# Kernel tuning notes

Hardware: AMD Instinct MI355X
Metric: run time of the kernel (lower is better)

Reference implementation:

```python
import jax, jax.numpy as jnp
import numpy as np
import math

N, T, D, H = 64, 128, 512, 1024

def setup_inputs() -> dict:
    key = jax.random.key(0)
    ks = jax.random.split(key, 5)
    x = jax.random.normal(ks[0], (N, T, D), dtype=jnp.float32)
    A = jax.random.normal(ks[1], (N, H, 4, 4), dtype=jnp.float32)
    Wx = jax.random.normal(ks[2], (D, 4 * H), dtype=jnp.float32) / math.sqrt(D)
    Wh = jax.random.normal(ks[3], (H, 4 * H), dtype=jnp.float32) / math.sqrt(H)
    Wattn = jax.random.normal(ks[4], (H, 4 * H), dtype=jnp.float32) / math.sqrt(H)
    b = jnp.zeros((4 * H,), dtype=jnp.float32)
    return {"x": x, "A": A, "Wx": Wx, "Wh": Wh, "Wattn": Wattn, "b": b}

def reference(x, A, Wx, Wh, Wattn, b):
    n, t, d = x.shape
    h_dim = A.shape[1]
    L = A.shape[2] * A.shape[3]  # 16 spatial locations
    Af = A.reshape(n, h_dim, L)                      # (N, H, 16)
    h0 = jnp.mean(Af, axis=-1)                       # mean over 4x4 -> (N, H)
    c0 = h0
    inv_sqrt_h = 1.0 / math.sqrt(h_dim)

    def step(carry, xt):
        prev_h, prev_c = carry
        # scaled dot-product attention over 16 locations
        scores = jnp.einsum('nh,nhl->nl', prev_h, Af) * inv_sqrt_h  # (N, 16)
        w = jax.nn.softmax(scores, axis=1)
        attn = jnp.einsum('nhl,nl->nh', Af, w)                      # (N, H)
        # LSTM gates
        a = xt @ Wx + prev_h @ Wh + attn @ Wattn + b                # (N, 4H)
        i, f, o, g = jnp.split(a, 4, axis=1)
        i, f, o = jax.nn.sigmoid(i), jax.nn.sigmoid(f), jax.nn.sigmoid(o)
        g = jnp.tanh(g)
        next_c = f * prev_c + i * g
        next_h = o * jnp.tanh(next_c)
        return (next_h, next_c), next_h

    xs = jnp.swapaxes(x, 0, 1)                       # (T, N, D)
    _, hs = jax.lax.scan(step, (h0, c0), xs)         # hs: (T, N, H)
    return jnp.swapaxes(hs, 0, 1)                    # (N, T, H)
```

## Files before the change

kernel.cpp:

```cpp
#include <hip/hip_runtime.h>
#include <stdint.h>


#define Tt 128
#define FH 4096
#define RING_D 32

typedef __bf16 bf8 __attribute__((ext_vector_type(8)));
typedef float f4 __attribute__((ext_vector_type(4)));
typedef short s8v __attribute__((ext_vector_type(8)));
typedef unsigned long long ull;

__device__ __forceinline__ float bf2f(unsigned short u) {
    union { unsigned u32; float f; } x; x.u32 = ((unsigned)u) << 16; return x.f;
}
__device__ __forceinline__ unsigned short f2bf(float f) {
    union { float f32; unsigned u; } x; x.f32 = f;
    unsigned r = x.u + 0x7fffu + ((x.u >> 16) & 1u);
    return (unsigned short)(r >> 16);
}
__device__ __forceinline__ ull ald(const ull* p) {
    return __hip_atomic_load((ull*)p, __ATOMIC_RELAXED, __HIP_MEMORY_SCOPE_AGENT);
}
__device__ __forceinline__ void ast(ull* p, ull v) {
    __hip_atomic_store(p, v, __ATOMIC_RELAXED, __HIP_MEMORY_SCOPE_AGENT);
}
__device__ __forceinline__ int aldi(const int* p) {
    return __hip_atomic_load((int*)p, __ATOMIC_RELAXED, __HIP_MEMORY_SCOPE_AGENT);
}
__device__ __forceinline__ void asti(int* p, int v) {
    __hip_atomic_store(p, v, __ATOMIC_RELAXED, __HIP_MEMORY_SCOPE_AGENT);
}


__global__ __launch_bounds__(256) void k_cast_bf16(const float* __restrict__ in,
                                                   unsigned short* __restrict__ out, int n) {
    int i = blockIdx.x * 256 + threadIdx.x;
    if (i < n) out[i] = f2bf(in[i]);
}

__global__ __launch_bounds__(256) void k_transpose_bf16(const float* __restrict__ W,
                                                        unsigned short* __restrict__ WT, int K) {
    __shared__ float tl[32][33];
    int c0 = blockIdx.x * 32, k0 = blockIdx.y * 32;
    int tx = threadIdx.x & 31, ty = threadIdx.x >> 5;
    #pragma unroll
    for (int i = 0; i < 32; i += 8) tl[ty + i][tx] = W[(size_t)(k0 + ty + i) * 4096 + c0 + tx];
    __syncthreads();
    #pragma unroll
    for (int i = 0; i < 32; i += 8) WT[(size_t)(c0 + ty + i) * K + k0 + tx] = f2bf(tl[tx][ty + i]);
}

__global__ __launch_bounds__(256) void k_afl(const float* __restrict__ A,
                                             unsigned short* __restrict__ Afl) {
    int idx = blockIdx.x * 256 + threadIdx.x;
    int k = idx & 1023, l = (idx >> 10) & 15, n = idx >> 14;
    Afl[idx] = f2bf(A[((size_t)n * 1024 + k) * 16 + l]);
}

__global__ __launch_bounds__(256) void k_init(const float* __restrict__ A,
                                              float* __restrict__ cstate,
                                              unsigned short* __restrict__ ring0) {
    int idx = blockIdx.x * 256 + threadIdx.x;
    const float* ap = A + (size_t)idx * 16;
    float s = 0.f;
    #pragma unroll
    for (int l = 0; l < 16; l++) s += ap[l];
    float h = s * (1.0f / 16.0f);
    cstate[idx] = h;
    ring0[idx] = f2bf(h);
}

__global__ __launch_bounds__(256) void k_gemm(const unsigned short* __restrict__ A,
                                              const unsigned short* __restrict__ BT,
                                              const float* __restrict__ bias,
                                              unsigned short* __restrict__ out,
                                              int M, int Nn, int K, int mode) {
    __shared__ unsigned short As[128][40];
    __shared__ unsigned short Bs[128][40];
    int m0 = blockIdx.y * 128, n0 = blockIdx.x * 128;
    int tid = threadIdx.x, lane = tid & 63, wave = tid >> 6;
    int wr = wave >> 1, wc = wave & 1, quad = lane >> 4, l16 = lane & 15;
    f4 acc[4][4];
    #pragma unroll
    for (int i = 0; i < 4; i++)
        #pragma unroll
        for (int j = 0; j < 4; j++) acc[i][j] = f4{0.f, 0.f, 0.f, 0.f};

    for (int k0 = 0; k0 < K; k0 += 32) {
        __syncthreads();
        #pragma unroll
        for (int i = 0; i < 2; i++) {
            int idx = i * 256 + tid, r = idx >> 2, c = idx & 3;
            *(s8v*)&As[r][c * 8] = *(const s8v*)&A[(size_t)(m0 + r) * K + k0 + c * 8];
            *(s8v*)&Bs[r][c * 8] = *(const s8v*)&BT[(size_t)(n0 + r) * K + k0 + c * 8];
        }
        __syncthreads();
        bf8 af[4], bfr[4];
        #pragma unroll
        for (int i = 0; i < 4; i++) af[i] = *(const bf8*)&As[wr * 64 + i * 16 + l16][quad * 8];
        #pragma unroll
        for (int j = 0; j < 4; j++) bfr[j] = *(const bf8*)&Bs[wc * 64 + j * 16 + l16][quad * 8];
        #pragma unroll
        for (int i = 0; i < 4; i++)
            #pragma unroll
            for (int j = 0; j < 4; j++)
                acc[i][j] = __builtin_amdgcn_mfma_f32_16x16x32_bf16(af[i], bfr[j], acc[i][j], 0, 0, 0);
    }

    #pragma unroll
    for (int i = 0; i < 4; i++)
        #pragma unroll
        for (int j = 0; j < 4; j++) {
            int row0 = m0 + wr * 64 + i * 16 + quad * 4;
            int col = n0 + wc * 64 + j * 16 + l16;
            float bia = bias ? bias[col] : 0.0f;
            int jj = col & 1023, g = col >> 10;
            #pragma unroll
            for (int r = 0; r < 4; r++) {
                float v = acc[i][j][r] + bia;
                int rw = row0 + r;
                if (mode == 0) {
                    out[(size_t)rw * Nn + col] = f2bf(v);
                } else if (mode == 1) {
                    int n = rw >> 4, l = rw & 15;
                    out[(((size_t)n * 1024 + jj) * 4 + g) * 16 + l] = f2bf(v);
                } else {
                    int n = rw >> 7, t = rw & 127;
                    out[(((size_t)t * 64 + n) * 1024 + jj) * 4 + g] = f2bf(v);
                }
            }
        }
}

__global__ __launch_bounds__(512, 2) void k_recur(
    const unsigned short* __restrict__ Afl,
    const unsigned short* __restrict__ WhT, const unsigned short* __restrict__ xwx,
    const unsigned short* __restrict__ P2, const float* __restrict__ cstate,
    unsigned short* __restrict__ ring,
    ull* __restrict__ wE,
    int* __restrict__ hflag,
    float* __restrict__ out) {
    __shared__ unsigned short WhS[32][1024];
    __shared__ unsigned short hS[32][1024];
    __shared__ float aL[32][36];
    __shared__ float wL[512];
    __shared__ float sL[4][16];
    __shared__ unsigned short hpk[32][8];

    const int wid = blockIdx.x;
    const int R = wid >> 7, C = wid & 127;
    const int tid = threadIdx.x, lane = tid & 63, wave = tid >> 6;
    const int l16 = lane & 15, quad = lane >> 4;

    const int ntile = wave & 1, ctile = (wave >> 1) & 1;
    const int n_l = tid >> 3, j = tid & 7;
    const int n_glob = R * 32 + n_l;
    const int jcol = C * 8 + j;
    const bool sduty = (C < 32) && (wave >= 4);
    const int skg = wave - 4;
    const int sn = R * 32 + C;

    for (int c = tid; c < 4096; c += 512) {
        int row = c >> 7, pos = c & 127;
        int q = row >> 3, jj = row & 7;
        int acolg = q * 1024 + C * 8 + jj;
        s8v v = *(const s8v*)&WhT[(size_t)acolg * 1024 + pos * 8];
        int e = (pos * 8) ^ ((row & 7) << 3);
        *(s8v*)&WhS[row][e] = v;
    }

    float creg = (tid < 256) ? cstate[(size_t)n_glob * 1024 + jcol] : 0.f;

    __syncthreads();

    for (int t = 0; t < Tt; ++t) {
        const unsigned short* rg = ring + (size_t)(t & (RING_D - 1)) * 65536;
        unsigned short* rw = ring + (size_t)((t + 1) & (RING_D - 1)) * 65536;

        ull xw8 = 0;
        s8v p2r[4][2];
        if (tid < 256) {
            xw8 = __builtin_nontemporal_load(
                (const ull*)xwx + ((size_t)t * 64 + n_glob) * 1024 + jcol);
            const s8v* pp = (const s8v*)(P2 + ((size_t)n_glob * 1024 + jcol) * 64);
            #pragma unroll
            for (int q = 0; q < 4; q++) {
                p2r[q][0] = pp[q * 2];
                p2r[q][1] = pp[q * 2 + 1];
            }
        }

        if (t > 0 && tid < 128) {
            while (aldi(&hflag[(R * 128 + tid) * 32]) < t)
                __builtin_amdgcn_s_sleep(2);
        }
        __syncthreads();
        __builtin_amdgcn_fence(__ATOMIC_ACQUIRE, "workgroup");

        #pragma unroll
        for (int it = 0; it < 8; ++it) {
            int c = it * 512 + tid;
            int row = c >> 7, pos = c & 127;
            s8v v = *(const s8v*)&rg[((size_t)(R * 32 + row)) * 1024 + pos * 8];
            int e = (pos * 8) ^ ((row & 7) << 3);
            *(s8v*)&hS[row][e] = v;
        }
        __syncthreads();

        if (wave < 4) {
            const int arow = ntile * 16 + l16;
            const int brow = ctile * 16 + l16;
            const int aswz = (arow & 7) << 3, bswz = (brow & 7) << 3;
            const int kb = quad * 8;
            f4 acc = {0.f, 0.f, 0.f, 0.f};
            #pragma unroll 8
            for (int ks = 0; ks < 32; ++ks) {
                bf8 a = *(const bf8*)&hS[arow][(kb + ks * 32) ^ aswz];
                bf8 b = *(const bf8*)&WhS[brow][(kb + ks * 32) ^ bswz];
                acc = __builtin_amdgcn_mfma_f32_16x16x32_bf16(a, b, acc, 0, 0, 0);
            }
            #pragma unroll
            for (int r = 0; r < 4; r++)
                aL[ntile * 16 + quad * 4 + r][ctile * 16 + l16] = acc[r];
        } else if (sduty) {
            const int sl = lane & 15, kq = lane >> 4;
            const int swz = (C & 7) << 3;
            const unsigned short* ap = Afl + ((size_t)sn * 16 + sl) * 1024
                                       + skg * 256 + kq * 64;
            float psum = 0.f;
            #pragma unroll
            for (int kc = 0; kc < 8; ++kc) {
                int kbase = skg * 256 + kq * 64 + kc * 8;
                s8v hv = *(const s8v*)&hS[C][kbase ^ swz];
                s8v av = *(const s8v*)&ap[kc * 8];
                #pragma unroll
                for (int e2 = 0; e2 < 8; e2++)
                    psum = fmaf(bf2f((unsigned short)hv[e2]),
                                bf2f((unsigned short)av[e2]), psum);
            }
            psum += __shfl_xor(psum, 16, 64);
            psum += __shfl_xor(psum, 32, 64);
            if (lane < 16) sL[skg][sl] = psum;
        }
        __syncthreads();

        if (C < 32 && tid < 16) {
            float s = (sL[0][tid] + sL[1][tid] + sL[2][tid] + sL[3][tid])
                      * (1.0f / 32.0f);
            float m = s;
            m = fmaxf(m, __shfl_xor(m, 1, 64));
            m = fmaxf(m, __shfl_xor(m, 2, 64));
            m = fmaxf(m, __shfl_xor(m, 4, 64));
            m = fmaxf(m, __shfl_xor(m, 8, 64));
            float e = __expf(s - m);
            float sum = e;
            sum += __shfl_xor(sum, 1, 64);
            sum += __shfl_xor(sum, 2, 64);
            sum += __shfl_xor(sum, 4, 64);
            sum += __shfl_xor(sum, 8, 64);
            union { ull u; unsigned v[2]; } pk;
            union { float f; unsigned b; } wb; wb.f = e / sum;
            pk.v[0] = wb.b;
            pk.v[1] = (unsigned)(t + 1);
            ast(&wE[(size_t)sn * 16 + tid], pk.u);
        }

        if (tid < 256) {
            const size_t wb = (size_t)n_glob * 16 + j * 2;
            ull a0, a1;
            for (;;) {
                a0 = ald(&wE[wb]);
                a1 = ald(&wE[wb + 1]);
                if ((unsigned)(a0 >> 32) >= (unsigned)(t + 1) &&
                    (unsigned)(a1 >> 32) >= (unsigned)(t + 1)) break;
                __builtin_amdgcn_s_sleep(2);
            }
            union { unsigned b; float f; } w0, w1;
            w0.b = (unsigned)a0; w1.b = (unsigned)a1;
            wL[tid * 2] = w0.f; wL[tid * 2 + 1] = w1.f;
        }
        __syncthreads();

        if (tid < 256) {
            float av4[4];
            #pragma unroll
            for (int q = 0; q < 4; q++) {
                int al = q * 8 + j;
                float v = aL[n_l][al] + bf2f((unsigned short)(xw8 >> (16 * q)));
                float sa = 0.f;
                #pragma unroll
                for (int l = 0; l < 8; l++)
                    sa = fmaf(wL[n_l * 16 + l], bf2f((unsigned short)p2r[q][0][l]), sa);
                #pragma unroll
                for (int l = 0; l < 8; l++)
                    sa = fmaf(wL[n_l * 16 + 8 + l], bf2f((unsigned short)p2r[q][1][l]), sa);
                av4[q] = v + sa;
            }
            float ig = 1.f / (1.f + __expf(-av4[0]));
            float fg = 1.f / (1.f + __expf(-av4[1]));
            float og = 1.f / (1.f + __expf(-av4[2]));
            float gg = tanhf(av4[3]);
            creg = fg * creg + ig * gg;
            float hv = og * tanhf(creg);
            out[((size_t)n_glob * Tt + t) * 1024 + jcol] = hv;
            hpk[n_l][j] = f2bf(hv);
        }
        __syncthreads();

        if (t < Tt - 1) {
            if (tid < 64) {
                int row = tid >> 1, half = tid & 1;
                ull v = *(const ull*)&hpk[row][half * 4];
                ast((ull*)rw + ((size_t)(R * 32 + row) << 8) + C * 2 + half, v);
                asm volatile("s_waitcnt vmcnt(0)" ::: "memory");
                if (tid == 0) asti(&hflag[wid * 32], t + 1);
            }
        }
    }
}


extern "C" void kernel_launch(void* const* d_in, const int* in_sizes, int n_in,
                              void* d_out, int out_size, void* d_ws, size_t ws_size,
                              hipStream_t stream) {
    const float* x     = (const float*)d_in[0];
    const float* A     = (const float*)d_in[1];
    const float* Wx    = (const float*)d_in[2];
    const float* Wh    = (const float*)d_in[3];
    const float* Wattn = (const float*)d_in[4];
    const float* b     = (const float*)d_in[5];
    float* out = (float*)d_out;
    char* ws = (char*)d_ws;

    unsigned short* xbf    = (unsigned short*)(ws);
    unsigned short* P2     = (unsigned short*)(ws);
    unsigned short* WxT    = (unsigned short*)(ws + 8388608);
    unsigned short* WhT    = (unsigned short*)(ws + 12582912);
    unsigned short* WattnT = (unsigned short*)(ws + 20971520);
    unsigned short* ring   = (unsigned short*)(ws + 20971520);
    unsigned short* Afl    = (unsigned short*)(ws + 29360128);
    unsigned short* xwx    = (unsigned short*)(ws + 31457280);
    float* cstate          = (float*)(ws + 98566144);
    ull* wE                = (ull*)(ws + 98828288);
    int* hflag             = (int*)(ws + 99094528);

    (void)hipMemsetAsync(ws + 98828288, 0, 8192, stream);
    (void)hipMemsetAsync(ws + 99094528, 0, 32768, stream);

    k_cast_bf16<<<16384, 256, 0, stream>>>(x, xbf, 4194304);
    k_transpose_bf16<<<dim3(128, 16), 256, 0, stream>>>(Wx, WxT, 512);
    k_transpose_bf16<<<dim3(128, 32), 256, 0, stream>>>(Wh, WhT, 1024);
    k_transpose_bf16<<<dim3(128, 32), 256, 0, stream>>>(Wattn, WattnT, 1024);
    k_afl<<<4096, 256, 0, stream>>>(A, Afl);

    k_gemm<<<dim3(32, 64), 256, 0, stream>>>(xbf, WxT, b, xwx, 8192, 4096, 512, 2);
    k_gemm<<<dim3(32, 8), 256, 0, stream>>>(Afl, WattnT, nullptr, P2, 1024, 4096, 1024, 1);

    k_init<<<256, 256, 0, stream>>>(A, cstate, ring);

    k_recur<<<256, 512, 0, stream>>>(Afl, WhT, xwx, P2, cstate, ring, wE,
                                     hflag, out);
}
```

Before: 1.076 ms.

## Move softmax to consumers and drop per-step barriers via shuffles

Score-producing waves now publish raw partial attention scores directly, four locations per wave. Each consumer thread computes the softmax itself with wave shuffles, which removes the score-combining stage, the weight staging in shared memory and two block barriers per timestep. The new hidden state is packed into 64-bit stores with lane shuffles instead of going through shared memory, and a single barrier precedes the flag publish. The softmax work is duplicated across consumer threads. The flag publish also drops the explicit wait for outstanding stores, which relies on the barrier and the release store for ordering.

```diff
diff --git a/kernel.cpp b/kernel.cpp
--- a/kernel.cpp
+++ b/kernel.cpp
@@ -144,9 +144,6 @@
     __shared__ unsigned short WhS[32][1024];
     __shared__ unsigned short hS[32][1024];
     __shared__ float aL[32][36];
-    __shared__ float wL[512];
-    __shared__ float sL[4][16];
-    __shared__ unsigned short hpk[32][8];
 
     const int wid = blockIdx.x;
     const int R = wid >> 7, C = wid & 127;
@@ -224,47 +221,37 @@
             for (int r = 0; r < 4; r++)
                 aL[ntile * 16 + quad * 4 + r][ctile * 16 + l16] = acc[r];
         } else if (sduty) {
-            const int sl = lane & 15, kq = lane >> 4;
+            const int sl4 = lane & 3;
+            const int kq = lane >> 2;
+            const int l_glob = skg * 4 + sl4;
             const int swz = (C & 7) << 3;
-            const unsigned short* ap = Afl + ((size_t)sn * 16 + sl) * 1024
-                                       + skg * 256 + kq * 64;
+            const unsigned short* ap = Afl + ((size_t)sn * 16 + l_glob) * 1024
+                                       + kq * 64;
             float psum = 0.f;
             #pragma unroll
             for (int kc = 0; kc < 8; ++kc) {
-                int kbase = skg * 256 + kq * 64 + kc * 8;
+                int c8 = (kc + kq) & 7;
+                int kbase = kq * 64 + c8 * 8;
                 s8v hv = *(const s8v*)&hS[C][kbase ^ swz];
-                s8v av = *(const s8v*)&ap[kc * 8];
+                s8v av = *(const s8v*)&ap[c8 * 8];
                 #pragma unroll
                 for (int e2 = 0; e2 < 8; e2++)
                     psum = fmaf(bf2f((unsigned short)hv[e2]),
                                 bf2f((unsigned short)av[e2]), psum);
             }
+            psum += __shfl_xor(psum, 4, 64);
+            psum += __shfl_xor(psum, 8, 64);
             psum += __shfl_xor(psum, 16, 64);
             psum += __shfl_xor(psum, 32, 64);
-            if (lane < 16) sL[skg][sl] = psum;
-        }
-        __syncthreads();
-
-        if (C < 32 && tid < 16) {
-            float s = (sL[0][tid] + sL[1][tid] + sL[2][tid] + sL[3][tid])
-                      * (1.0f / 32.0f);
-            float m = s;
-            m = fmaxf(m, __shfl_xor(m, 1, 64));
-            m = fmaxf(m, __shfl_xor(m, 2, 64));
-            m = fmaxf(m, __shfl_xor(m, 4, 64));
-            m = fmaxf(m, __shfl_xor(m, 8, 64));
-            float e = __expf(s - m);
-            float sum = e;
-            sum += __shfl_xor(sum, 1, 64);
-            sum += __shfl_xor(sum, 2, 64);
-            sum += __shfl_xor(sum, 4, 64);
-            sum += __shfl_xor(sum, 8, 64);
-            union { ull u; unsigned v[2]; } pk;
-            union { float f; unsigned b; } wb; wb.f = e / sum;
-            pk.v[0] = wb.b;
-            pk.v[1] = (unsigned)(t + 1);
-            ast(&wE[(size_t)sn * 16 + tid], pk.u);
-        }
+            if (lane < 4) {
+                union { ull u; unsigned v[2]; } pk;
+                union { float f; unsigned b; } wb; wb.f = psum;
+                pk.v[0] = wb.b;
+                pk.v[1] = (unsigned)(t + 1);
+                ast(&wE[(size_t)sn * 16 + skg * 4 + lane], pk.u);
+            }
+        }
+        __syncthreads();
 
         if (tid < 256) {
             const size_t wb = (size_t)n_glob * 16 + j * 2;
@@ -276,25 +263,39 @@
                     (unsigned)(a1 >> 32) >= (unsigned)(t + 1)) break;
                 __builtin_amdgcn_s_sleep(2);
             }
-            union { unsigned b; float f; } w0, w1;
-            w0.b = (unsigned)a0; w1.b = (unsigned)a1;
-            wL[tid * 2] = w0.f; wL[tid * 2 + 1] = w1.f;
-        }
-        __syncthreads();
-
-        if (tid < 256) {
+            union { unsigned b; float f; } r0, r1;
+            r0.b = (unsigned)a0; r1.b = (unsigned)a1;
+            float s0 = r0.f * (1.0f / 32.0f);
+            float s1 = r1.f * (1.0f / 32.0f);
+            float m = fmaxf(s0, s1);
+            m = fmaxf(m, __shfl_xor(m, 1, 64));
+            m = fmaxf(m, __shfl_xor(m, 2, 64));
+            m = fmaxf(m, __shfl_xor(m, 4, 64));
+            float e0 = __expf(s0 - m), e1 = __expf(s1 - m);
+            float sm = e0 + e1;
+            sm += __shfl_xor(sm, 1, 64);
+            sm += __shfl_xor(sm, 2, 64);
+            sm += __shfl_xor(sm, 4, 64);
+            float inv = 1.0f / sm;
+            float w0 = e0 * inv, w1 = e1 * inv;
+            const int base = lane & 56;
+            float wv[16];
+            #pragma unroll
+            for (int mth = 0; mth < 8; mth++) {
+                wv[2 * mth]     = __shfl(w0, base + mth, 64);
+                wv[2 * mth + 1] = __shfl(w1, base + mth, 64);
+            }
             float av4[4];
             #pragma unroll
             for (int q = 0; q < 4; q++) {
-                int al = q * 8 + j;
-                float v = aL[n_l][al] + bf2f((unsigned short)(xw8 >> (16 * q)));
+                float v = aL[n_l][q * 8 + j] + bf2f((unsigned short)(xw8 >> (16 * q)));
                 float sa = 0.f;
                 #pragma unroll
                 for (int l = 0; l < 8; l++)
-                    sa = fmaf(wL[n_l * 16 + l], bf2f((unsigned short)p2r[q][0][l]), sa);
+                    sa = fmaf(wv[l], bf2f((unsigned short)p2r[q][0][l]), sa);
                 #pragma unroll
                 for (int l = 0; l < 8; l++)
-                    sa = fmaf(wL[n_l * 16 + 8 + l], bf2f((unsigned short)p2r[q][1][l]), sa);
+                    sa = fmaf(wv[8 + l], bf2f((unsigned short)p2r[q][1][l]), sa);
                 av4[q] = v + sa;
             }
             float ig = 1.f / (1.f + __expf(-av4[0]));
@@ -304,19 +305,18 @@
             creg = fg * creg + ig * gg;
             float hv = og * tanhf(creg);
             out[((size_t)n_glob * Tt + t) * 1024 + jcol] = hv;
-            hpk[n_l][j] = f2bf(hv);
-        }
-        __syncthreads();
-
-        if (t < Tt - 1) {
-            if (tid < 64) {
-                int row = tid >> 1, half = tid & 1;
-                ull v = *(const ull*)&hpk[row][half * 4];
-                ast((ull*)rw + ((size_t)(R * 32 + row) << 8) + C * 2 + half, v);
-                asm volatile("s_waitcnt vmcnt(0)" ::: "memory");
-                if (tid == 0) asti(&hflag[wid * 32], t + 1);
-            }
-        }
+            int hvi = (int)f2bf(hv);
+            int h1 = __shfl(hvi, lane + 1, 64);
+            int h2 = __shfl(hvi, lane + 2, 64);
+            int h3 = __shfl(hvi, lane + 3, 64);
+            if (t < Tt - 1 && (j & 3) == 0) {
+                ull u = (ull)(unsigned)(hvi | (h1 << 16))
+                      | ((ull)(unsigned)(h2 | (h3 << 16)) << 32);
+                ast((ull*)rw + (((size_t)(R * 32 + n_l)) << 8) + C * 2 + (j >> 2), u);
+            }
+        }
+        __syncthreads();
+        if (t < Tt - 1 && tid == 0) asti(&hflag[wid * 32], t + 1);
     }
 }
 
```

Result: slower. 1.111 ms (+3.3%).

## Split recurrent h wait and load into halves to overlap MFMA with second-half fetch

Applied to the files above, without the earlier changes.

Each step now waits only on the producers of the first half of h columns and loads that half into shared memory. The MFMA waves then run the first half of the K loop while waves 6-7 wait for and load the second half. The score-partial work is also split across the two phases. The intent is to overlap the cross-workgroup synchronization and global h loads with matrix compute, at the cost of an extra block barrier per step.

```diff
diff --git a/kernel.cpp b/kernel.cpp
--- a/kernel.cpp
+++ b/kernel.cpp
@@ -157,8 +157,6 @@
     const int n_l = tid >> 3, j = tid & 7;
     const int n_glob = R * 32 + n_l;
     const int jcol = C * 8 + j;
-    const bool sduty = (C < 32) && (wave >= 4);
-    const int skg = wave - 4;
     const int sn = R * 32 + C;
 
     for (int c = tid; c < 4096; c += 512) {
@@ -191,7 +189,7 @@
             }
         }
 
-        if (t > 0 && tid < 128) {
+        if (t > 0 && tid < 64) {
             while (aldi(&hflag[(R * 128 + tid) * 32]) < t)
                 __builtin_amdgcn_s_sleep(2);
         }
@@ -199,31 +197,77 @@
         __builtin_amdgcn_fence(__ATOMIC_ACQUIRE, "workgroup");
 
         #pragma unroll
-        for (int it = 0; it < 8; ++it) {
+        for (int it = 0; it < 4; ++it) {
             int c = it * 512 + tid;
-            int row = c >> 7, pos = c & 127;
+            int row = c >> 6, pos = c & 63;
             s8v v = *(const s8v*)&rg[((size_t)(R * 32 + row)) * 1024 + pos * 8];
             int e = (pos * 8) ^ ((row & 7) << 3);
             *(s8v*)&hS[row][e] = v;
         }
         __syncthreads();
 
+        f4 acc = {0.f, 0.f, 0.f, 0.f};
+        const int arow = ntile * 16 + l16;
+        const int brow = ctile * 16 + l16;
+        const int aswz = (arow & 7) << 3, bswz = (brow & 7) << 3;
+        const int kb = quad * 8;
         if (wave < 4) {
-            const int arow = ntile * 16 + l16;
-            const int brow = ctile * 16 + l16;
-            const int aswz = (arow & 7) << 3, bswz = (brow & 7) << 3;
-            const int kb = quad * 8;
-            f4 acc = {0.f, 0.f, 0.f, 0.f};
             #pragma unroll 8
-            for (int ks = 0; ks < 32; ++ks) {
+            for (int ks = 0; ks < 16; ++ks) {
                 bf8 a = *(const bf8*)&hS[arow][(kb + ks * 32) ^ aswz];
                 bf8 b = *(const bf8*)&WhS[brow][(kb + ks * 32) ^ bswz];
                 acc = __builtin_amdgcn_mfma_f32_16x16x32_bf16(a, b, acc, 0, 0, 0);
             }
+        } else if (wave >= 6) {
+            if (t > 0) {
+                while (aldi(&hflag[(R * 128 + 64 + lane) * 32]) < t)
+                    __builtin_amdgcn_s_sleep(2);
+            }
+            __builtin_amdgcn_fence(__ATOMIC_ACQUIRE, "workgroup");
+            const int tb = (wave - 6) * 64 + lane;
+            #pragma unroll
+            for (int it = 0; it < 16; ++it) {
+                int c2 = it * 128 + tb;
+                int row = c2 >> 6, pos = 64 + (c2 & 63);
+                s8v v = *(const s8v*)&rg[((size_t)(R * 32 + row)) * 1024 + pos * 8];
+                int e = (pos * 8) ^ ((row & 7) << 3);
+                *(s8v*)&hS[row][e] = v;
+            }
+        } else if (C < 32) {
+            const int skg = wave - 4;
+            const int sl = lane & 15, kq = lane >> 4;
+            const int swz = (C & 7) << 3;
+            const unsigned short* ap = Afl + ((size_t)sn * 16 + sl) * 1024
+                                       + skg * 256 + kq * 64;
+            float psum = 0.f;
+            #pragma unroll
+            for (int kc = 0; kc < 8; ++kc) {
+                int kbase = skg * 256 + kq * 64 + kc * 8;
+                s8v hv = *(const s8v*)&hS[C][kbase ^ swz];
+                s8v av = *(const s8v*)&ap[kc * 8];
+                #pragma unroll
+                for (int e2 = 0; e2 < 8; e2++)
+                    psum = fmaf(bf2f((unsigned short)hv[e2]),
+                                bf2f((unsigned short)av[e2]), psum);
+            }
+            psum += __shfl_xor(psum, 16, 64);
+            psum += __shfl_xor(psum, 32, 64);
+            if (lane < 16) sL[skg][sl] = psum;
+        }
+        __syncthreads();
+
+        if (wave < 4) {
+            #pragma unroll 8
+            for (int ks = 16; ks < 32; ++ks) {
+                bf8 a = *(const bf8*)&hS[arow][(kb + ks * 32) ^ aswz];
+                bf8 b = *(const bf8*)&WhS[brow][(kb + ks * 32) ^ bswz];
+                acc = __builtin_amdgcn_mfma_f32_16x16x32_bf16(a, b, acc, 0, 0, 0);
+            }
             #pragma unroll
             for (int r = 0; r < 4; r++)
                 aL[ntile * 16 + quad * 4 + r][ctile * 16 + l16] = acc[r];
-        } else if (sduty) {
+        } else if (wave >= 6 && C < 32) {
+            const int skg = wave - 4;
             const int sl = lane & 15, kq = lane >> 4;
             const int swz = (C & 7) << 3;
             const unsigned short* ap = Afl + ((size_t)sn * 16 + sl) * 1024
@@ -286,8 +330,7 @@
             float av4[4];
             #pragma unroll
             for (int q = 0; q < 4; q++) {
-                int al = q * 8 + j;
-                float v = aL[n_l][al] + bf2f((unsigned short)(xw8 >> (16 * q)));
+                float v = aL[n_l][q * 8 + j] + bf2f((unsigned short)(xw8 >> (16 * q)));
                 float sa = 0.f;
                 #pragma unroll
                 for (int l = 0; l < 8; l++)
```

Result: faster. 1.004 ms (median of 2 runs) (-6.7%).
